# Performance work log

Measured on AMD Instinct MI355X. Metric: run time of the kernel, lower is better.

The kernel has to match this reference:

```python
import jax, jax.numpy as jnp
import numpy as np

TAU = 2.0
V_TH = 1.0
ALPHA = 2.0  # ATan surrogate alpha

@jax.custom_vjp
def spike_fn(x):
    return (x >= 0.0).astype(x.dtype)

def _spike_fwd(x):
    return spike_fn(x), x

def _spike_bwd(x, g):
    # spikingjelly ATan surrogate: alpha/2 / (1 + (pi/2*alpha*x)^2)
    return (g * (ALPHA / 2.0) / (1.0 + (jnp.pi / 2.0 * ALPHA * x) ** 2),)

spike_fn.defvjp(_spike_fwd, _spike_bwd)

def lif_step(v, h):
    # decay_input=True, v_reset=0: v += (h - v)/tau
    v = v + (h - v) / TAU
    s = spike_fn(v - V_TH)
    v = v * (1.0 - s)  # hard reset to v_reset=0
    return v, s

def setup_inputs() -> dict:
    key = jax.random.key(0)
    k1, k2, k3 = jax.random.split(key, 3)
    B, T, I, H, O = 128, 2048, 128, 1024, 128
    x = jax.random.normal(k1, (B, T, I), dtype=jnp.float32)
    W1 = jax.random.normal(k2, (H, I), dtype=jnp.float32) / np.sqrt(I)
    b1 = jnp.zeros((H,), dtype=jnp.float32)
    W2 = jax.random.normal(k3, (O, H), dtype=jnp.float32) / np.sqrt(H)
    b2 = jnp.zeros((O,), dtype=jnp.float32)
    return {"x": x, "W1": W1, "b1": b1, "W2": W2, "b2": b2}

def reference(x, W1, b1, W2, b2):
    B, T, I = x.shape
    H = W1.shape[0]
    O = W2.shape[0]
    xt = jnp.transpose(x, (1, 0, 2))  # [T, B, I]

    def step(carry, x_t):
        v1, v2 = carry
        h1 = x_t @ W1.T + b1
        v1, s1 = lif_step(v1, h1)
        h2 = s1 @ W2.T + b2
        v2, s2 = lif_step(v2, h2)
        return (v1, v2), s2

    v1_0 = jnp.zeros((B, H), dtype=x.dtype)
    v2_0 = jnp.zeros((B, O), dtype=x.dtype)
    _, outs = jax.lax.scan(step, (v1_0, v2_0), xt)  # [T, B, O]
    decision_start = T // 2
    return jnp.sum(outs[decision_start:], axis=0)  # [B, O]
```

## Files before the change

kernel.cpp:

```cpp
#include <hip/hip_runtime.h>
#include <stdint.h>

#define NB 128
#define NT 2048
#define NI 128
#define NH 1024
#define NO 128

__global__ __launch_bounds__(256) void w2t_kernel(
    const float* __restrict__ W2, float* __restrict__ W2T)
{
    const int idx = blockIdx.x * 256 + threadIdx.x;
    const int o = idx >> 10;
    const int k = idx & 1023;
    W2T[(size_t)k * NO + o] = W2[idx];
}

__global__ __launch_bounds__(256, 4) void snn_phaseA(
    const float* __restrict__ x, const float* __restrict__ W1,
    const float* __restrict__ b1, uint64_t* __restrict__ s1bits)
{
    const int b = blockIdx.x >> 3;
    const int htile = blockIdx.x & 7;
    const int tid = threadIdx.x;
    const int wv = tid >> 6;
    const int lane = tid & 63;
    const int kh = wv >> 1;
    const int hl = ((wv & 1) << 6) | lane;
    const int h = (htile << 7) | hl;

    float wk[64];
#pragma unroll
    for (int j = 0; j < 64; ++j)
        wk[j] = W1[(size_t)h * NI + (kh << 6) + j];
    const float bias = b1[h];

    __shared__ float red[2][128];

    const int koff = __builtin_amdgcn_readfirstlane(kh << 6);
    const float* __restrict__ xb = x + (size_t)b * NT * NI + koff;

    float v = 0.0f;
    for (int t = 0; t < NT; ++t) {
        const float* __restrict__ xr = xb + (size_t)t * NI;
        float a0 = 0.f, a1 = 0.f, a2 = 0.f, a3 = 0.f;
#pragma unroll
        for (int j = 0; j < 64; j += 4) {
            a0 = fmaf(xr[j + 0], wk[j + 0], a0);
            a1 = fmaf(xr[j + 1], wk[j + 1], a1);
            a2 = fmaf(xr[j + 2], wk[j + 2], a2);
            a3 = fmaf(xr[j + 3], wk[j + 3], a3);
        }
        const float partial = (a0 + a1) + (a2 + a3);
        if (kh) red[t & 1][hl] = partial;
        __syncthreads();
        if (!kh) {
            const float h1 = partial + red[t & 1][hl] + bias;
            v = fmaf(h1 - v, 0.5f, v);
            const bool sp = (v >= 1.0f);
            v = sp ? 0.0f : v;
            const unsigned long long m = __ballot(sp);
            if (lane == 0)
                s1bits[((size_t)t * NB + b) * (NH / 64) + (htile << 1) + (wv & 1)] =
                    (uint64_t)m;
        }
    }
}

__global__ __launch_bounds__(256, 4) void snn_phaseB(
    const uint64_t* __restrict__ s1bits, const float* __restrict__ W2T,
    float* __restrict__ h2)
{
    const int mtile = blockIdx.x;
    const int wv = threadIdx.x >> 6;
    const int lane = threadIdx.x & 63;
    const int o0 = __builtin_amdgcn_readfirstlane(wv << 5);
    const int m0 = (mtile << 7) + lane;

    float acc0[32], acc1[32];
#pragma unroll
    for (int i = 0; i < 32; ++i) { acc0[i] = 0.f; acc1[i] = 0.f; }

    const uint32_t* __restrict__ sp0 =
        (const uint32_t*)(s1bits + (size_t)m0 * (NH / 64));
    const uint32_t* __restrict__ sp1 =
        (const uint32_t*)(s1bits + (size_t)(m0 + 64) * (NH / 64));
    const float* __restrict__ wbase = W2T + o0;

    for (int kw = 0; kw < NH / 32; ++kw) {
        const uint32_t w0 = sp0[kw];
        const uint32_t w1 = sp1[kw];
        const float* __restrict__ wr = wbase + (size_t)(kw << 5) * NO;
#pragma unroll
        for (int kj = 0; kj < 32; ++kj) {
            const float f0 = (float)((w0 >> kj) & 1u);
            const float f1 = (float)((w1 >> kj) & 1u);
            const float* __restrict__ wrow = wr + (size_t)kj * NO;
#pragma unroll
            for (int oo = 0; oo < 32; ++oo) {
                const float w = wrow[oo];
                acc0[oo] = fmaf(f0, w, acc0[oo]);
                acc1[oo] = fmaf(f1, w, acc1[oo]);
            }
        }
    }

    float* __restrict__ p0 = h2 + (size_t)m0 * NO + o0;
    float* __restrict__ p1 = h2 + (size_t)(m0 + 64) * NO + o0;
#pragma unroll
    for (int oo = 0; oo < 32; ++oo) p0[oo] = acc0[oo];
#pragma unroll
    for (int oo = 0; oo < 32; ++oo) p1[oo] = acc1[oo];
}

__global__ __launch_bounds__(256) void snn_phaseD(
    const float* __restrict__ h2, const float* __restrict__ b2,
    float* __restrict__ out)
{
    const int idx = blockIdx.x * 256 + threadIdx.x;
    const int b = idx >> 7;
    const int o = idx & 127;
    const float bias = b2[o];

    const float* __restrict__ pa = h2 + (size_t)b * NO + o;
    const float* __restrict__ pb = h2 + (size_t)(b + 64) * NO + o;
    float va = 0.f, vb = 0.f, ca = 0.f, cb = 0.f;
#pragma unroll 8
    for (int t = 0; t < NT; ++t) {
        const float ha = pa[(size_t)t * NB * NO] + bias;
        const float hb = pb[(size_t)t * NB * NO] + bias;
        va = fmaf(ha - va, 0.5f, va);
        vb = fmaf(hb - vb, 0.5f, vb);
        const bool sa = (va >= 1.0f);
        const bool sb = (vb >= 1.0f);
        va = sa ? 0.f : va;
        vb = sb ? 0.f : vb;
        if (t >= NT / 2) {
            ca += sa ? 1.f : 0.f;
            cb += sb ? 1.f : 0.f;
        }
    }
    out[(size_t)b * NO + o] = ca;
    out[(size_t)(b + 64) * NO + o] = cb;
}

extern "C" void kernel_launch(void* const* d_in, const int* in_sizes, int n_in,
                              void* d_out, int out_size, void* d_ws,
                              size_t ws_size, hipStream_t stream)
{
    const float* x  = (const float*)d_in[0];
    const float* W1 = (const float*)d_in[1];
    const float* b1 = (const float*)d_in[2];
    const float* W2 = (const float*)d_in[3];
    const float* b2 = (const float*)d_in[4];
    float* out = (float*)d_out;

    uint8_t* ws = (uint8_t*)d_ws;
    uint64_t* s1bits = (uint64_t*)ws;
    float* W2T = (float*)(ws + (size_t)NT * NB * (NH / 64) * 8);
    float* h2 = (float*)(ws + (size_t)NT * NB * (NH / 64) * 8 +
                         (size_t)NH * NO * 4);

    w2t_kernel<<<dim3((NH * NO) / 256), dim3(256), 0, stream>>>(W2, W2T);
    snn_phaseA<<<dim3(NB * 8), dim3(256), 0, stream>>>(x, W1, b1, s1bits);
    snn_phaseB<<<dim3((NT * NB) / 128), dim3(256), 0, stream>>>(s1bits, W2T, h2);
    snn_phaseD<<<dim3((NB / 2 * NO) / 256), dim3(256), 0, stream>>>(h2, b2, out);
}
```

Measured before the change: 2.493 ms.

## Use sparse spike-driven gather for layer 2 and full-K rows in layer 1

Layer-1 now gives each thread all 128 input weights in registers, loaded as dwordx4. This removes the LDS reduction and the per-timestep __syncthreads, though it halves occupancy. Layer-2 no longer does a dense bit-masked FMA matmul; each wave walks the set bits of the spike mask and accumulates only the matching W2 rows from a repacked float2 layout, so work scales with spike sparsity. The LIF readout kernel uses one neuron per thread for more parallelism. The dynamic loop in the layer-2 gather is serial per wave and adds branching cost if spikes are dense.

```diff
diff --git a/kernel.cpp b/kernel.cpp
--- a/kernel.cpp
+++ b/kernel.cpp
@@ -7,110 +7,103 @@
 #define NH 1024
 #define NO 128
 
-__global__ __launch_bounds__(256) void w2t_kernel(
-    const float* __restrict__ W2, float* __restrict__ W2T)
+typedef float f32x4 __attribute__((ext_vector_type(4)));
+
+__global__ __launch_bounds__(256) void w2p_kernel(
+    const float* __restrict__ W2, float2* __restrict__ W2P)
 {
     const int idx = blockIdx.x * 256 + threadIdx.x;
-    const int o = idx >> 10;
-    const int k = idx & 1023;
-    W2T[(size_t)k * NO + o] = W2[idx];
+    const int k = idx >> 6;
+    const int j = idx & 63;
+    W2P[idx] = make_float2(W2[(size_t)j * NH + k], W2[(size_t)(j + 64) * NH + k]);
 }
 
-__global__ __launch_bounds__(256, 4) void snn_phaseA(
+__global__ __launch_bounds__(256, 2) void snn_phaseA(
     const float* __restrict__ x, const float* __restrict__ W1,
     const float* __restrict__ b1, uint64_t* __restrict__ s1bits)
 {
-    const int b = blockIdx.x >> 3;
-    const int htile = blockIdx.x & 7;
-    const int tid = threadIdx.x;
-    const int wv = tid >> 6;
-    const int lane = tid & 63;
-    const int kh = wv >> 1;
-    const int hl = ((wv & 1) << 6) | lane;
-    const int h = (htile << 7) | hl;
+    const int b = blockIdx.x >> 2;
+    const int htile = blockIdx.x & 3;
+    const int wv = threadIdx.x >> 6;
+    const int lane = threadIdx.x & 63;
+    const int h = (htile << 8) | (wv << 6) | lane;
 
-    float wk[64];
+    f32x4 w[32];
+    const float* wp = W1 + (size_t)h * NI;
 #pragma unroll
-    for (int j = 0; j < 64; ++j)
-        wk[j] = W1[(size_t)h * NI + (kh << 6) + j];
+    for (int i = 0; i < 32; ++i) {
+        asm volatile("global_load_dwordx4 %0, %1, off"
+                     : "=v"(w[i])
+                     : "v"(wp + i * 4));
+    }
+    asm volatile("s_waitcnt vmcnt(0)"
+                 : "+v"(w[0]), "+v"(w[1]), "+v"(w[2]), "+v"(w[3]),
+                   "+v"(w[4]), "+v"(w[5]), "+v"(w[6]), "+v"(w[7]),
+                   "+v"(w[8]), "+v"(w[9]), "+v"(w[10]), "+v"(w[11]),
+                   "+v"(w[12]), "+v"(w[13]), "+v"(w[14]), "+v"(w[15]),
+                   "+v"(w[16]), "+v"(w[17]), "+v"(w[18]), "+v"(w[19]),
+                   "+v"(w[20]), "+v"(w[21]), "+v"(w[22]), "+v"(w[23]),
+                   "+v"(w[24]), "+v"(w[25]), "+v"(w[26]), "+v"(w[27]),
+                   "+v"(w[28]), "+v"(w[29]), "+v"(w[30]), "+v"(w[31])
+                 :
+                 : "memory");
+    __builtin_amdgcn_sched_barrier(0);
+
     const float bias = b1[h];
-
-    __shared__ float red[2][128];
-
-    const int koff = __builtin_amdgcn_readfirstlane(kh << 6);
-    const float* __restrict__ xb = x + (size_t)b * NT * NI + koff;
+    const float* __restrict__ xb = x + (size_t)b * NT * NI;
 
     float v = 0.0f;
     for (int t = 0; t < NT; ++t) {
-        const float* __restrict__ xr = xb + (size_t)t * NI;
+        const f32x4* __restrict__ xr =
+            (const f32x4*)(xb + (size_t)t * NI);
         float a0 = 0.f, a1 = 0.f, a2 = 0.f, a3 = 0.f;
 #pragma unroll
-        for (int j = 0; j < 64; j += 4) {
-            a0 = fmaf(xr[j + 0], wk[j + 0], a0);
-            a1 = fmaf(xr[j + 1], wk[j + 1], a1);
-            a2 = fmaf(xr[j + 2], wk[j + 2], a2);
-            a3 = fmaf(xr[j + 3], wk[j + 3], a3);
+        for (int i = 0; i < 32; ++i) {
+            const f32x4 xv = xr[i];
+            a0 = fmaf(xv.x, w[i].x, a0);
+            a1 = fmaf(xv.y, w[i].y, a1);
+            a2 = fmaf(xv.z, w[i].z, a2);
+            a3 = fmaf(xv.w, w[i].w, a3);
         }
-        const float partial = (a0 + a1) + (a2 + a3);
-        if (kh) red[t & 1][hl] = partial;
-        __syncthreads();
-        if (!kh) {
-            const float h1 = partial + red[t & 1][hl] + bias;
-            v = fmaf(h1 - v, 0.5f, v);
-            const bool sp = (v >= 1.0f);
-            v = sp ? 0.0f : v;
-            const unsigned long long m = __ballot(sp);
-            if (lane == 0)
-                s1bits[((size_t)t * NB + b) * (NH / 64) + (htile << 1) + (wv & 1)] =
-                    (uint64_t)m;
-        }
+        const float h1 = ((a0 + a1) + (a2 + a3)) + bias;
+        v = fmaf(h1 - v, 0.5f, v);
+        const bool sp = (v >= 1.0f);
+        v = sp ? 0.0f : v;
+        const unsigned long long m = __ballot(sp);
+        if (lane == 0)
+            s1bits[((size_t)t * NB + b) * (NH / 64) + (htile << 2) + wv] =
+                (uint64_t)m;
     }
 }
 
 __global__ __launch_bounds__(256, 4) void snn_phaseB(
-    const uint64_t* __restrict__ s1bits, const float* __restrict__ W2T,
+    const uint64_t* __restrict__ s1bits, const float2* __restrict__ W2P,
     float* __restrict__ h2)
 {
-    const int mtile = blockIdx.x;
     const int wv = threadIdx.x >> 6;
     const int lane = threadIdx.x & 63;
-    const int o0 = __builtin_amdgcn_readfirstlane(wv << 5);
-    const int m0 = (mtile << 7) + lane;
+    const size_t m = (size_t)blockIdx.x * 4 + wv;
 
-    float acc0[32], acc1[32];
-#pragma unroll
-    for (int i = 0; i < 32; ++i) { acc0[i] = 0.f; acc1[i] = 0.f; }
+    const uint64_t* __restrict__ sb = s1bits + m * (NH / 64);
+    float a0 = 0.f, a1 = 0.f;
 
-    const uint32_t* __restrict__ sp0 =
-        (const uint32_t*)(s1bits + (size_t)m0 * (NH / 64));
-    const uint32_t* __restrict__ sp1 =
-        (const uint32_t*)(s1bits + (size_t)(m0 + 64) * (NH / 64));
-    const float* __restrict__ wbase = W2T + o0;
-
-    for (int kw = 0; kw < NH / 32; ++kw) {
-        const uint32_t w0 = sp0[kw];
-        const uint32_t w1 = sp1[kw];
-        const float* __restrict__ wr = wbase + (size_t)(kw << 5) * NO;
-#pragma unroll
-        for (int kj = 0; kj < 32; ++kj) {
-            const float f0 = (float)((w0 >> kj) & 1u);
-            const float f1 = (float)((w1 >> kj) & 1u);
-            const float* __restrict__ wrow = wr + (size_t)kj * NO;
-#pragma unroll
-            for (int oo = 0; oo < 32; ++oo) {
-                const float w = wrow[oo];
-                acc0[oo] = fmaf(f0, w, acc0[oo]);
-                acc1[oo] = fmaf(f1, w, acc1[oo]);
-            }
+#pragma unroll 1
+    for (int wd = 0; wd < NH / 64; ++wd) {
+        const uint64_t m64 = sb[wd];
+        const uint32_t mlo = (uint32_t)__builtin_amdgcn_readfirstlane((int)(uint32_t)m64);
+        const uint32_t mhi = (uint32_t)__builtin_amdgcn_readfirstlane((int)(uint32_t)(m64 >> 32));
+        uint64_t msk = ((uint64_t)mhi << 32) | mlo;
+        while (msk) {
+            const int i = __builtin_ctzll(msk);
+            msk &= (msk - 1);
+            const size_t k = ((size_t)wd << 6) + i;
+            const float2 ww = W2P[k * 64 + lane];
+            a0 += ww.x;
+            a1 += ww.y;
         }
     }
-
-    float* __restrict__ p0 = h2 + (size_t)m0 * NO + o0;
-    float* __restrict__ p1 = h2 + (size_t)(m0 + 64) * NO + o0;
-#pragma unroll
-    for (int oo = 0; oo < 32; ++oo) p0[oo] = acc0[oo];
-#pragma unroll
-    for (int oo = 0; oo < 32; ++oo) p1[oo] = acc1[oo];
+    h2[m * NO + lane] = a0;
+    h2[m * NO + 64 + lane] = a1;
 }
 
 __global__ __launch_bounds__(256) void snn_phaseD(
@@ -122,26 +115,17 @@
     const int o = idx & 127;
     const float bias = b2[o];
 
-    const float* __restrict__ pa = h2 + (size_t)b * NO + o;
-    const float* __restrict__ pb = h2 + (size_t)(b + 64) * NO + o;
-    float va = 0.f, vb = 0.f, ca = 0.f, cb = 0.f;
+    const float* __restrict__ p = h2 + (size_t)b * NO + o;
+    float v = 0.f, c = 0.f;
 #pragma unroll 8
     for (int t = 0; t < NT; ++t) {
-        const float ha = pa[(size_t)t * NB * NO] + bias;
-        const float hb = pb[(size_t)t * NB * NO] + bias;
-        va = fmaf(ha - va, 0.5f, va);
-        vb = fmaf(hb - vb, 0.5f, vb);
-        const bool sa = (va >= 1.0f);
-        const bool sb = (vb >= 1.0f);
-        va = sa ? 0.f : va;
-        vb = sb ? 0.f : vb;
-        if (t >= NT / 2) {
-            ca += sa ? 1.f : 0.f;
-            cb += sb ? 1.f : 0.f;
-        }
+        const float hh = p[(size_t)t * NB * NO] + bias;
+        v = fmaf(hh - v, 0.5f, v);
+        const bool s = (v >= 1.0f);
+        v = s ? 0.f : v;
+        if (t >= NT / 2) c += s ? 1.f : 0.f;
     }
-    out[(size_t)b * NO + o] = ca;
-    out[(size_t)(b + 64) * NO + o] = cb;
+    out[idx] = c;
 }
 
 extern "C" void kernel_launch(void* const* d_in, const int* in_sizes, int n_in,
@@ -157,12 +141,12 @@
 
     uint8_t* ws = (uint8_t*)d_ws;
     uint64_t* s1bits = (uint64_t*)ws;
-    float* W2T = (float*)(ws + (size_t)NT * NB * (NH / 64) * 8);
+    float2* W2P = (float2*)(ws + (size_t)NT * NB * (NH / 64) * 8);
     float* h2 = (float*)(ws + (size_t)NT * NB * (NH / 64) * 8 +
-                         (size_t)NH * NO * 4);
+                         (size_t)NH * 64 * sizeof(float2));
 
-    w2t_kernel<<<dim3((NH * NO) / 256), dim3(256), 0, stream>>>(W2, W2T);
-    snn_phaseA<<<dim3(NB * 8), dim3(256), 0, stream>>>(x, W1, b1, s1bits);
-    snn_phaseB<<<dim3((NT * NB) / 128), dim3(256), 0, stream>>>(s1bits, W2T, h2);
-    snn_phaseD<<<dim3((NB / 2 * NO) / 256), dim3(256), 0, stream>>>(h2, b2, out);
+    w2p_kernel<<<dim3((NH * 64) / 256), dim3(256), 0, stream>>>(W2, W2P);
+    snn_phaseA<<<dim3(NB * 4), dim3(256), 0, stream>>>(x, W1, b1, s1bits);
+    snn_phaseB<<<dim3((NT * NB) / 4), dim3(256), 0, stream>>>(s1bits, W2P, h2);
+    snn_phaseD<<<dim3((NB * NO) / 256), dim3(256), 0, stream>>>(h2, b2, out);
 }
```

Measured after the change: 3.543 ms. +42.1%, slower.
